# Kernel optimization log

Hardware: AMD Instinct MI355X
Metric: run time of the kernel (lower is better)

The kernel has to match this reference:

```python
import jax, jax.numpy as jnp
import numpy as np

N, IN1, IN2, OUT, DX, DY = 32, 4, 4, 128, 128, 128


def setup_inputs() -> dict:
    key = jax.random.key(0)
    k = jax.random.split(key, 6)
    x = jax.random.normal(k[0], (N, IN1, DX), dtype=jnp.float32)
    y = jax.random.normal(k[1], (N, IN2, DY), dtype=jnp.float32)
    # kernel_C: [out_channels, in1*in2]
    C = jax.random.normal(k[2], (OUT, IN1 * IN2), dtype=jnp.float32) * 0.1
    # one Conv1d pair (kernel_size=3 -> only j=1: k=2, dilation=2, padding=1)
    W_A = jax.random.normal(k[3], (OUT, IN1 * IN2, 2), dtype=jnp.float32) * 0.1
    W_B = jax.random.normal(k[4], (OUT, IN1 * IN2, 2), dtype=jnp.float32) * 0.1
    bias = jax.random.uniform(k[5], (OUT,), dtype=jnp.float32, minval=-0.5, maxval=0.5)
    return {"x": x, "y": y, "C": C, "W_A": W_A, "W_B": W_B, "bias": bias}


def _dilated_conv(inp, w):
    # PyTorch Conv1d(kernel_size=2, stride=1, padding=1, dilation=2, bias=False)
    return jax.lax.conv_general_dilated(
        inp, w, window_strides=(1,), padding=[(1, 1)], rhs_dilation=(2,),
        dimension_numbers=("NCH", "OIH", "NCH"))


def reference(x, y, C, W_A, W_B, bias):
    n, in1, dx = x.shape
    _, in2, dy = y.shape
    out_ch = C.shape[0]
    # batch_cross_product: channel c = c1*in2 + c2 of outer product, then einsum with C.
    # Fused form (same math, no [N, in1*dx, in2*dy] intermediate):
    Cr = C.reshape(out_ch, in1, in2)
    bcp = jnp.einsum("nci,ndj,ocd->noij", x, y, Cr)  # [N, out, dx, dy]
    # x.repeat(1, in2, 1) / y.repeat(1, in1, 1) == tile along channel dim
    xA = jnp.tile(x, (1, in2, 1))  # [N, in1*in2, dx]
    yB = jnp.tile(y, (1, in1, 1))  # [N, in1*in2, dy]
    a = _dilated_conv(xA, W_A)  # [N, out, dx]
    b = _dilated_conv(yB, W_B)  # [N, out, dy]
    out = bcp + a[:, :, :, None] + b[:, :, None, :]
    return out + bias[None, :, None, None]
```

## Files before the change

### kernel.cpp

```cpp
#include <hip/hip_runtime.h>


__global__ __launch_bounds__(256) void scvc_kernel(
    const float* __restrict__ x,
    const float* __restrict__ y,
    const float* __restrict__ C,
    const float* __restrict__ WA,
    const float* __restrict__ WB,
    const float* __restrict__ bias,
    float* __restrict__ out)
{
    const int n    = blockIdx.x >> 7;
    const int o    = blockIdx.x & 127;
    const int tid  = threadIdx.x;
    const int wave = tid >> 6;
    const int lane = tid & 63;
    const int half = lane >> 5;
    const int col4 = (lane & 31) << 2;
    const int r0   = wave << 5;

    const float* xb = x + (n << 9);
    const float* yb = y + (n << 9);

    float cr[4][4];
    #pragma unroll
    for (int c = 0; c < 4; ++c) {
        #pragma unroll
        for (int d = 0; d < 4; ++d)
            cr[c][d] = C[o * 16 + c * 4 + d];
    }
    float wam[4], wap[4], wbm[4], wbp[4];
    #pragma unroll
    for (int c = 0; c < 4; ++c) {
        float sa0 = 0.f, sa1 = 0.f, sb0 = 0.f, sb1 = 0.f;
        #pragma unroll
        for (int r = 0; r < 4; ++r) {
            sa0 += WA[o * 32 + (4 * r + c) * 2 + 0];
            sa1 += WA[o * 32 + (4 * r + c) * 2 + 1];
            sb0 += WB[o * 32 + (4 * r + c) * 2 + 0];
            sb1 += WB[o * 32 + (4 * r + c) * 2 + 1];
        }
        wam[c] = sa0; wap[c] = sa1; wbm[c] = sb0; wbp[c] = sb1;
    }
    const float bo = bias[o];

    const float cm = (col4 > 0)   ? 1.f : 0.f;
    const float cp = (col4 < 124) ? 1.f : 0.f;
    const int   jm = (col4 > 0)   ? col4 - 1 : 0;
    const int   jp = (col4 < 124) ? col4 + 4 : 0;

    float yr[4][4];
    float bj0 = bo, bj1 = bo, bj2 = bo, bj3 = bo;
    #pragma unroll
    for (int d = 0; d < 4; ++d) {
        const float4 v = *(const float4*)(yb + (d << 7) + col4);
        yr[d][0] = v.x; yr[d][1] = v.y; yr[d][2] = v.z; yr[d][3] = v.w;
        const float ymv = yb[(d << 7) + jm] * cm;
        const float ypv = yb[(d << 7) + jp] * cp;
        bj0 = fmaf(ymv,     wbm[d], bj0); bj0 = fmaf(v.y, wbp[d], bj0);
        bj1 = fmaf(v.x,     wbm[d], bj1); bj1 = fmaf(v.z, wbp[d], bj1);
        bj2 = fmaf(v.y,     wbm[d], bj2); bj2 = fmaf(v.w, wbp[d], bj2);
        bj3 = fmaf(v.z,     wbm[d], bj3); bj3 = fmaf(ypv, wbp[d], bj3);
    }

    float* op = out + ((long)blockIdx.x << 14) + (r0 << 7) + (half << 7) + col4;

    #pragma unroll 4
    for (int it = 0; it < 16; ++it) {
        const int i = r0 + (it << 1) + half;
        const int im = (i > 0)   ? i - 1 : 0;
        const int ip = (i < 127) ? i + 1 : 127;
        const float mm = (i > 0)   ? 1.f : 0.f;
        const float mp = (i < 127) ? 1.f : 0.f;

        float t40 = 0.f, t41 = 0.f, t42 = 0.f, t43 = 0.f;
        float am = 0.f, ap = 0.f;
        #pragma unroll
        for (int c = 0; c < 4; ++c) {
            const float xc = xb[(c << 7) + i];
            t40 = fmaf(xc, cr[c][0], t40);
            t41 = fmaf(xc, cr[c][1], t41);
            t42 = fmaf(xc, cr[c][2], t42);
            t43 = fmaf(xc, cr[c][3], t43);
            am  = fmaf(xb[(c << 7) + im], wam[c], am);
            ap  = fmaf(xb[(c << 7) + ip], wap[c], ap);
        }
        const float a = mm * am + mp * ap;

        float4 r;
        r.x = t40 * yr[0][0] + t41 * yr[1][0] + t42 * yr[2][0] + t43 * yr[3][0] + (a + bj0);
        r.y = t40 * yr[0][1] + t41 * yr[1][1] + t42 * yr[2][1] + t43 * yr[3][1] + (a + bj1);
        r.z = t40 * yr[0][2] + t41 * yr[1][2] + t42 * yr[2][2] + t43 * yr[3][2] + (a + bj2);
        r.w = t40 * yr[0][3] + t41 * yr[1][3] + t42 * yr[2][3] + t43 * yr[3][3] + (a + bj3);
        *(float4*)op = r;
        op += 256;
    }
}

extern "C" void kernel_launch(void* const* d_in, const int* in_sizes, int n_in,
                              void* d_out, int out_size, void* d_ws, size_t ws_size,
                              hipStream_t stream) {
    const float* x    = (const float*)d_in[0];
    const float* y    = (const float*)d_in[1];
    const float* C    = (const float*)d_in[2];
    const float* WA   = (const float*)d_in[3];
    const float* WB   = (const float*)d_in[4];
    const float* bias = (const float*)d_in[5];
    float* out = (float*)d_out;

    scvc_kernel<<<32 * 128, 256, 0, stream>>>(x, y, C, WA, WB, bias, out);
}
```

Baseline: 281.4 us.

## Precompute per-row and per-column terms in shared memory before the output loop

Measured after the change: 263.0 us. -6.5%, faster.

```diff
diff --git a/kernel.cpp b/kernel.cpp
--- a/kernel.cpp
+++ b/kernel.cpp
@@ -19,8 +19,19 @@
     const int col4 = (lane & 31) << 2;
     const int r0   = wave << 5;
 
+    __shared__ float t4[128][4];
+    __shared__ float arow[128];
+    __shared__ float bcol[128];
+
     const float* xb = x + (n << 9);
     const float* yb = y + (n << 9);
+
+    float yr[4][4];
+    #pragma unroll
+    for (int d = 0; d < 4; ++d) {
+        const float4 v = *(const float4*)(yb + (d << 7) + col4);
+        yr[d][0] = v.x; yr[d][1] = v.y; yr[d][2] = v.z; yr[d][3] = v.w;
+    }
 
     float cr[4][4];
     #pragma unroll
@@ -44,54 +55,57 @@
     }
     const float bo = bias[o];
 
-    const float cm = (col4 > 0)   ? 1.f : 0.f;
-    const float cp = (col4 < 124) ? 1.f : 0.f;
-    const int   jm = (col4 > 0)   ? col4 - 1 : 0;
-    const int   jp = (col4 < 124) ? col4 + 4 : 0;
+    if (tid < 128) {
+        const int i = tid;
+        float xv[4], xm[4], xp[4];
+        #pragma unroll
+        for (int c = 0; c < 4; ++c) {
+            xv[c] = xb[(c << 7) + i];
+            xm[c] = (i > 0)   ? xb[(c << 7) + i - 1] : 0.f;
+            xp[c] = (i < 127) ? xb[(c << 7) + i + 1] : 0.f;
+        }
+        #pragma unroll
+        for (int d = 0; d < 4; ++d) {
+            float s = 0.f;
+            #pragma unroll
+            for (int c = 0; c < 4; ++c) s = fmaf(xv[c], cr[c][d], s);
+            t4[i][d] = s;
+        }
+        float a = 0.f;
+        #pragma unroll
+        for (int c = 0; c < 4; ++c) {
+            a = fmaf(xm[c], wam[c], a);
+            a = fmaf(xp[c], wap[c], a);
+        }
+        arow[i] = a;
+    } else {
+        const int j = tid - 128;
+        float b = bo;
+        #pragma unroll
+        for (int c = 0; c < 4; ++c) {
+            const float ym = (j > 0)   ? yb[(c << 7) + j - 1] : 0.f;
+            const float yp = (j < 127) ? yb[(c << 7) + j + 1] : 0.f;
+            b = fmaf(ym, wbm[c], b);
+            b = fmaf(yp, wbp[c], b);
+        }
+        bcol[j] = b;
+    }
+    __syncthreads();
 
-    float yr[4][4];
-    float bj0 = bo, bj1 = bo, bj2 = bo, bj3 = bo;
-    #pragma unroll
-    for (int d = 0; d < 4; ++d) {
-        const float4 v = *(const float4*)(yb + (d << 7) + col4);
-        yr[d][0] = v.x; yr[d][1] = v.y; yr[d][2] = v.z; yr[d][3] = v.w;
-        const float ymv = yb[(d << 7) + jm] * cm;
-        const float ypv = yb[(d << 7) + jp] * cp;
-        bj0 = fmaf(ymv,     wbm[d], bj0); bj0 = fmaf(v.y, wbp[d], bj0);
-        bj1 = fmaf(v.x,     wbm[d], bj1); bj1 = fmaf(v.z, wbp[d], bj1);
-        bj2 = fmaf(v.y,     wbm[d], bj2); bj2 = fmaf(v.w, wbp[d], bj2);
-        bj3 = fmaf(v.z,     wbm[d], bj3); bj3 = fmaf(ypv, wbp[d], bj3);
-    }
+    const float4 bv = *(const float4*)(&bcol[col4]);
+    const float bj0 = bv.x, bj1 = bv.y, bj2 = bv.z, bj3 = bv.w;
 
     float* op = out + ((long)blockIdx.x << 14) + (r0 << 7) + (half << 7) + col4;
-
-    #pragma unroll 4
+    #pragma unroll
     for (int it = 0; it < 16; ++it) {
         const int i = r0 + (it << 1) + half;
-        const int im = (i > 0)   ? i - 1 : 0;
-        const int ip = (i < 127) ? i + 1 : 127;
-        const float mm = (i > 0)   ? 1.f : 0.f;
-        const float mp = (i < 127) ? 1.f : 0.f;
-
-        float t40 = 0.f, t41 = 0.f, t42 = 0.f, t43 = 0.f;
-        float am = 0.f, ap = 0.f;
-        #pragma unroll
-        for (int c = 0; c < 4; ++c) {
-            const float xc = xb[(c << 7) + i];
-            t40 = fmaf(xc, cr[c][0], t40);
-            t41 = fmaf(xc, cr[c][1], t41);
-            t42 = fmaf(xc, cr[c][2], t42);
-            t43 = fmaf(xc, cr[c][3], t43);
-            am  = fmaf(xb[(c << 7) + im], wam[c], am);
-            ap  = fmaf(xb[(c << 7) + ip], wap[c], ap);
-        }
-        const float a = mm * am + mp * ap;
-
+        const float4 t = *(const float4*)(&t4[i][0]);
+        const float ai = arow[i];
         float4 r;
-        r.x = t40 * yr[0][0] + t41 * yr[1][0] + t42 * yr[2][0] + t43 * yr[3][0] + (a + bj0);
-        r.y = t40 * yr[0][1] + t41 * yr[1][1] + t42 * yr[2][1] + t43 * yr[3][1] + (a + bj1);
-        r.z = t40 * yr[0][2] + t41 * yr[1][2] + t42 * yr[2][2] + t43 * yr[3][2] + (a + bj2);
-        r.w = t40 * yr[0][3] + t41 * yr[1][3] + t42 * yr[2][3] + t43 * yr[3][3] + (a + bj3);
+        r.x = t.x * yr[0][0] + t.y * yr[1][0] + t.z * yr[2][0] + t.w * yr[3][0] + (ai + bj0);
+        r.y = t.x * yr[0][1] + t.y * yr[1][1] + t.z * yr[2][1] + t.w * yr[3][1] + (ai + bj1);
+        r.z = t.x * yr[0][2] + t.y * yr[1][2] + t.z * yr[2][2] + t.w * yr[3][2] + (ai + bj2);
+        r.w = t.x * yr[0][3] + t.y * yr[1][3] + t.z * yr[2][3] + t.w * yr[3][3] + (ai + bj3);
         *(float4*)op = r;
         op += 256;
     }
```
